# Kernel optimization log

Hardware: AMD Instinct MI355X
Metric: run time of the kernel (lower is better)

## Reference

```python
import jax, jax.numpy as jnp
import numpy as np

B, NR, NG = 16, 96, 64
AF, BF = 98, 6
H, QM, MAXNB, DEPTH = 300, 160, 10, 4
P = 2048
F = 2 * H + QM          # 760
D0 = F + 10             # 770


def _graph_idx(k, batch, n, idx_max):
    # gather_nd style indices (batch_idx, neighbor_idx): [batch, n, MAXNB, 2]
    nbr = jax.random.randint(k, (batch, n, MAXNB), 0, idx_max)
    b = jnp.broadcast_to(jnp.arange(batch)[:, None, None], (batch, n, MAXNB))
    return jnp.stack([b, nbr], axis=-1)


def setup_inputs() -> dict:
    key = jax.random.key(0)
    ks = jax.random.split(key, 32)
    f32 = jnp.float32
    inp = {}
    inp['res_atom'] = jax.random.normal(ks[0], (B, NR, AF), f32)
    inp['res_bond'] = jax.random.normal(ks[1], (B, NR, BF), f32)
    inp['res_atom_graph'] = _graph_idx(ks[2], B, NR, NR)
    inp['res_bond_graph'] = _graph_idx(ks[3], B, NR, NR)
    inp['res_num_nbs'] = jax.random.randint(ks[4], (B, NR), 1, MAXNB + 1)
    inp['res_node_mask'] = jnp.ones((B, NR, 1), f32)
    inp['rg_atom'] = jax.random.normal(ks[5], (B, NG, AF), f32)
    inp['rg_bond'] = jax.random.normal(ks[6], (B, NG, BF), f32)
    inp['rg_atom_graph'] = _graph_idx(ks[7], B, NG, NG)
    inp['rg_bond_graph'] = _graph_idx(ks[8], B, NG, NG)
    inp['rg_num_nbs'] = jax.random.randint(ks[9], (B, NG), 1, MAXNB + 1)
    inp['rg_node_mask'] = jnp.ones((B, NG, 1), f32)
    seg = jnp.repeat(jnp.arange(B), P // B)  # sorted reaction ids for segment_mean
    i = jax.random.randint(ks[10], (P,), 0, NR)
    j = jax.random.randint(ks[11], (P,), 0, NR)
    inp['core_mask'] = jnp.stack([seg, i, j], axis=-1)[None]   # [1, P, 3]
    inp['fatom_qm'] = jax.random.normal(ks[12], (B, NR, QM), f32)
    inp['connect'] = jax.random.normal(ks[13], (1, P, 10), f32)
    STD = 0.1  # keep relu chains alive at depth 4
    w = lambda k, shape: STD * jax.random.normal(k, shape, f32)
    for pre, kk in (('res', 14), ('rg', 20)):
        inp[pre + '_W_atom'] = w(ks[kk], (AF, H))
        inp[pre + '_W_nei_atom'] = w(ks[kk + 1], (H, H))
        inp[pre + '_W_nei_bond'] = w(ks[kk + 2], (BF, H))
        inp[pre + '_W_self'] = w(ks[kk + 3], (H, H))
        inp[pre + '_W_U2'] = w(ks[kk + 4], (H + BF, H))
        inp[pre + '_W_U1'] = w(ks[kk + 5], (2 * H, H))
    inp['W_att_h'] = w(ks[26], (H, H))
    inp['W_att_s'] = w(ks[27], (H, 1))
    inp['W_score0'] = 0.01 * jax.random.normal(ks[28], (D0, D0), f32)
    inp['W_score'] = 0.01 * jax.random.normal(ks[29], (D0, 1), f32)
    return inp


def _wln(atom, bond, atom_graph, bond_graph, num_nbs, node_mask,
         W_atom, W_nei_atom, W_nei_bond, W_self, W_U2, W_U1):
    relu = jax.nn.relu
    af = relu(atom @ W_atom)                                       # [B,N,H]
    mask = (jnp.arange(MAXNB)[None, None, :] < num_nbs[:, :, None])
    mask = mask.astype(af.dtype)[..., None]                        # [B,N,MAXNB,1]
    for _ in range(DEPTH):
        fa = af[atom_graph[..., 0], atom_graph[..., 1]]            # [B,N,MAXNB,H]
        fb = bond[bond_graph[..., 0], bond_graph[..., 1]]          # [B,N,MAXNB,BF]
        h_nei = relu(fa @ W_nei_atom) * relu(fb @ W_nei_bond)
        f_nei = jnp.sum(h_nei * mask, axis=2)                      # masked nbr sum
        kernels = f_nei * relu(af @ W_self) * node_mask
        pre = relu(jnp.concatenate([fa, fb], axis=3) @ W_U2)
        nei_label = jnp.sum(pre * mask, axis=2)
        af = relu(jnp.concatenate([af, nei_label], axis=2) @ W_U1)
    return kernels


def _forward(res_atom, res_bond, res_atom_graph, res_bond_graph, res_num_nbs, res_node_mask,
             rg_atom, rg_bond, rg_atom_graph, rg_bond_graph, rg_num_nbs, rg_node_mask,
             core_mask, fatom_qm, connect,
             res_W_atom, res_W_nei_atom, res_W_nei_bond, res_W_self, res_W_U2, res_W_U1,
             rg_W_atom, rg_W_nei_atom, rg_W_nei_bond, rg_W_self, rg_W_U2, rg_W_U1,
             W_att_h, W_att_s, W_score0, W_score):
    res_h = _wln(res_atom, res_bond, res_atom_graph, res_bond_graph, res_num_nbs, res_node_mask,
                 res_W_atom, res_W_nei_atom, res_W_nei_bond, res_W_self, res_W_U2, res_W_U1)
    rg_h = _wln(rg_atom, rg_bond, rg_atom_graph, rg_bond_graph, rg_num_nbs, rg_node_mask,
                rg_W_atom, rg_W_nei_atom, rg_W_nei_bond, rg_W_self, rg_W_U2, rg_W_U1)
    # Global attention: broadcast pairwise sum reactant x reagent atoms
    pair_att = res_h[:, :, None, :] + rg_h[:, None, :, :]          # [B,NR,NG,H]
    att = jax.nn.sigmoid(jax.nn.relu(pair_att @ W_att_h) @ W_att_s)
    ctx = jnp.sum(att * rg_h[:, None, :, :], axis=2)               # [B,NR,H]
    h = jnp.concatenate([res_h, ctx, fatom_qm], axis=-1)           # [B,NR,F]
    cm = core_mask[0]                                              # [P,3] = (b,i,j)
    # atom_pair[b,i,j] = h[b,i] + h[b,j]; gather only the core pairs (no N^2 tensor)
    pair = h[cm[:, 0], cm[:, 1]] + h[cm[:, 0], cm[:, 2]]           # [P,F]
    rh = jax.nn.relu(jnp.concatenate([pair, connect[0]], axis=-1) @ W_score0)
    seg = cm[:, 0]
    sums = jax.ops.segment_sum(rh, seg, num_segments=B)
    cnt = jax.ops.segment_sum(jnp.ones((P,), rh.dtype), seg, num_segments=B)
    mean = sums / cnt[:, None]                                     # segment_mean
    return mean @ W_score                                          # [B,1]


def reference(res_atom, res_bond, res_atom_graph, res_bond_graph, res_num_nbs, res_node_mask,
              rg_atom, rg_bond, rg_atom_graph, rg_bond_graph, rg_num_nbs, rg_node_mask,
              core_mask, fatom_qm, connect,
              res_W_atom, res_W_nei_atom, res_W_nei_bond, res_W_self, res_W_U2, res_W_U1,
              rg_W_atom, rg_W_nei_atom, rg_W_nei_bond, rg_W_self, rg_W_U2, rg_W_U1,
              W_att_h, W_att_s, W_score0, W_score):
    return _forward(res_atom, res_bond, res_atom_graph, res_bond_graph, res_num_nbs, res_node_mask,
                    rg_atom, rg_bond, rg_atom_graph, rg_bond_graph, rg_num_nbs, rg_node_mask,
                    core_mask, fatom_qm, connect,
                    res_W_atom, res_W_nei_atom, res_W_nei_bond, res_W_self, res_W_U2, res_W_U1,
                    rg_W_atom, rg_W_nei_atom, rg_W_nei_bond, rg_W_self, rg_W_U2, rg_W_U1,
                    W_att_h, W_att_s, W_score0, W_score)
```

## Files before the change

kernel.cpp:

```cpp
#include <hip/hip_runtime.h>


constexpr int cB = 16, cNR = 96, cNG = 64;
constexpr int cAF = 98, cBF = 6;
constexpr int cH = 300, cQM = 160, cMAXNB = 10, cDEPTH = 4;
constexpr int cP = 2048;
constexpr int cF = 2 * cH + cQM;
constexpr int cD0 = cF + 10;

constexpr int Mres = cB * cNR;
constexpr int Mrg  = cB * cNG;

typedef __attribute__((ext_vector_type(8))) short v8s;
typedef __attribute__((ext_vector_type(4))) float v4f;

__device__ inline unsigned short f2bf(float f) {
  unsigned u = __float_as_uint(f);
  u += 0x7FFF + ((u >> 16) & 1);
  return (unsigned short)(u >> 16);
}
__device__ inline float bf2f(unsigned short s) {
  return __uint_as_float(((unsigned)s) << 16);
}

struct PrepArg { const float* W; unsigned short* hiT; unsigned short* loT; int K; int N; int Kpad; };
struct PrepArgs { PrepArg a[16]; };

__global__ __launch_bounds__(256) void prep_k(PrepArgs pa)
{
  PrepArg p = pa.a[blockIdx.z];
  int idx = blockIdx.x * 256 + threadIdx.x;
  int total = p.N * p.Kpad;
  if (idx >= total) return;
  int n = idx / p.Kpad, k = idx - n * p.Kpad;
  float w = (k < p.K) ? p.W[(size_t)k * p.N + n] : 0.f;
  unsigned short h = f2bf(w);
  p.hiT[idx] = h;
  p.loT[idx] = f2bf(w - bf2f(h));
}

struct GArg {
  const float* A; const float* A2;
  const unsigned short* W1h; const unsigned short* W1l;
  const unsigned short* W2h; const unsigned short* W2l;
  float* C; int M; int K1; int Kp1; int K2; int Kp2; int act;
};
struct GArgs6 { GArg a[6]; };

#define MFMA __builtin_amdgcn_mfma_f32_16x16x32_bf16

__global__ __launch_bounds__(256) void gemm_mfma(GArgs6 ga, int N)
{
  GArg g = ga.a[blockIdx.z];
  int m0 = blockIdx.y * 64;
  if (m0 >= g.M) return;
  int n0 = blockIdx.x * 64;
  int nT = (g.Kp1 + g.Kp2) >> 5;

  __shared__ unsigned short Ah[2][64][40];
  __shared__ unsigned short Al[2][64][40];
  __shared__ unsigned short Bh[2][64][40];
  __shared__ unsigned short Bl[2][64][40];

  int tid = threadIdx.x;
  int sm = tid >> 2;
  int sk = (tid & 3) << 3;

  float areg[8];
  uint4 bh_reg, bl_reg;

  auto fetch = [&](int kv0) {
    int kv = kv0 + sk;
    const float* src; int kk, Klim;
    if (kv < g.Kp1) { src = g.A  + (size_t)(m0 + sm) * g.K1; kk = kv;          Klim = g.K1; }
    else            { src = g.A2 + (size_t)(m0 + sm) * g.K2; kk = kv - g.Kp1;  Klim = g.K2; }
    if (((Klim & 3) == 0) && kk + 7 < Klim) {
      float4 v0 = *(const float4*)(src + kk);
      float4 v1 = *(const float4*)(src + kk + 4);
      areg[0]=v0.x; areg[1]=v0.y; areg[2]=v0.z; areg[3]=v0.w;
      areg[4]=v1.x; areg[5]=v1.y; areg[6]=v1.z; areg[7]=v1.w;
    } else {
#pragma unroll
      for (int j = 0; j < 8; ++j) areg[j] = (kk + j < Klim) ? src[kk + j] : 0.f;
    }
    int gn = n0 + sm;
    if (gn < N) {
      const unsigned short *ph, *pl;
      if (kv < g.Kp1) { size_t o = (size_t)gn * g.Kp1 + kv;            ph = g.W1h + o; pl = g.W1l + o; }
      else            { size_t o = (size_t)gn * g.Kp2 + (kv - g.Kp1);  ph = g.W2h + o; pl = g.W2l + o; }
      bh_reg = *(const uint4*)ph;
      bl_reg = *(const uint4*)pl;
    } else {
      bh_reg = make_uint4(0,0,0,0); bl_reg = make_uint4(0,0,0,0);
    }
  };

  auto store = [&](int buf) {
    unsigned hs[8], ls[8];
#pragma unroll
    for (int j = 0; j < 8; ++j) {
      unsigned short h = f2bf(areg[j]);
      hs[j] = h;
      ls[j] = f2bf(areg[j] - bf2f(h));
    }
    uint4 hh, ll;
    hh.x = hs[0] | (hs[1] << 16); hh.y = hs[2] | (hs[3] << 16);
    hh.z = hs[4] | (hs[5] << 16); hh.w = hs[6] | (hs[7] << 16);
    ll.x = ls[0] | (ls[1] << 16); ll.y = ls[2] | (ls[3] << 16);
    ll.z = ls[4] | (ls[5] << 16); ll.w = ls[6] | (ls[7] << 16);
    *(uint4*)&Ah[buf][sm][sk] = hh;
    *(uint4*)&Al[buf][sm][sk] = ll;
    *(uint4*)&Bh[buf][sm][sk] = bh_reg;
    *(uint4*)&Bl[buf][sm][sk] = bl_reg;
  };

  int l = tid & 63, w = tid >> 6;
  int wm = (w >> 1) << 5, wn = (w & 1) << 5;
  int ar = wm + (l & 15), br = wn + (l & 15);
  int kc = (l >> 4) << 3;

  v4f acc00 = {0,0,0,0}, acc01 = {0,0,0,0}, acc10 = {0,0,0,0}, acc11 = {0,0,0,0};

  fetch(0); store(0); __syncthreads();
  for (int t = 0; t < nT; ++t) {
    if (t + 1 < nT) fetch((t + 1) << 5);
    int cur = t & 1;
    v8s ah0 = *(const v8s*)&Ah[cur][ar][kc];
    v8s ah1 = *(const v8s*)&Ah[cur][ar + 16][kc];
    v8s al0 = *(const v8s*)&Al[cur][ar][kc];
    v8s al1 = *(const v8s*)&Al[cur][ar + 16][kc];
    v8s bh0 = *(const v8s*)&Bh[cur][br][kc];
    v8s bh1 = *(const v8s*)&Bh[cur][br + 16][kc];
    v8s bl0 = *(const v8s*)&Bl[cur][br][kc];
    v8s bl1 = *(const v8s*)&Bl[cur][br + 16][kc];
    acc00 = MFMA(ah0, bh0, acc00, 0, 0, 0);
    acc00 = MFMA(ah0, bl0, acc00, 0, 0, 0);
    acc00 = MFMA(al0, bh0, acc00, 0, 0, 0);
    acc01 = MFMA(ah0, bh1, acc01, 0, 0, 0);
    acc01 = MFMA(ah0, bl1, acc01, 0, 0, 0);
    acc01 = MFMA(al0, bh1, acc01, 0, 0, 0);
    acc10 = MFMA(ah1, bh0, acc10, 0, 0, 0);
    acc10 = MFMA(ah1, bl0, acc10, 0, 0, 0);
    acc10 = MFMA(al1, bh0, acc10, 0, 0, 0);
    acc11 = MFMA(ah1, bh1, acc11, 0, 0, 0);
    acc11 = MFMA(ah1, bl1, acc11, 0, 0, 0);
    acc11 = MFMA(al1, bh1, acc11, 0, 0, 0);
    if (t + 1 < nT) store(cur ^ 1);
    __syncthreads();
  }

  int rbase = m0 + wm + ((l >> 4) << 2);
  int cbase = n0 + wn + (l & 15);
  auto wr = [&](v4f a, int fi, int fj) {
    int gn = cbase + fj * 16;
    if (gn >= N) return;
    float* Cp = g.C + (size_t)(rbase + fi * 16) * N + gn;
#pragma unroll
    for (int r = 0; r < 4; ++r) {
      float v = a[r];
      if (g.act) v = fmaxf(v, 0.f);
      Cp[(size_t)r * N] = v;
    }
  };
  wr(acc00, 0, 0); wr(acc01, 0, 1); wr(acc10, 1, 0); wr(acc11, 1, 1);
}

__global__ __launch_bounds__(256) void score_mfma_k(
    const float* __restrict__ h, const float* __restrict__ conn,
    const int* __restrict__ cm,
    const unsigned short* __restrict__ W0h, const unsigned short* __restrict__ W0l,
    const float* __restrict__ Wsc, float* __restrict__ pairsum)
{
  const int Kp = 800;
  const int nT = Kp >> 5;
  int m0 = blockIdx.y * 64;
  int n0 = blockIdx.x * 64;

  __shared__ unsigned short Ah[2][64][40];
  __shared__ unsigned short Al[2][64][40];
  __shared__ unsigned short Bh[2][64][40];
  __shared__ unsigned short Bl[2][64][40];

  int tid = threadIdx.x;
  int sm = tid >> 2;
  int sk = (tid & 3) << 3;

  int p = m0 + sm;
  int s3 = cm[p * 3 + 0];
  const float* h1 = h + (size_t)(s3 * cNR + cm[p * 3 + 1]) * cF;
  const float* h2 = h + (size_t)(s3 * cNR + cm[p * 3 + 2]) * cF;
  const float* cp = conn + (size_t)p * 10;

  float areg[8];
  uint4 bh_reg, bl_reg;

  auto fetch = [&](int kv0) {
    int kv = kv0 + sk;
    if (kv + 7 < cF) {
      float4 u = *(const float4*)(h1 + kv);
      float4 v = *(const float4*)(h2 + kv);
      float4 u2 = *(const float4*)(h1 + kv + 4);
      float4 v2 = *(const float4*)(h2 + kv + 4);
      areg[0]=u.x+v.x; areg[1]=u.y+v.y; areg[2]=u.z+v.z; areg[3]=u.w+v.w;
      areg[4]=u2.x+v2.x; areg[5]=u2.y+v2.y; areg[6]=u2.z+v2.z; areg[7]=u2.w+v2.w;
    } else {
#pragma unroll
      for (int j = 0; j < 8; ++j) {
        int k = kv + j;
        float v = 0.f;
        if (k < cF) v = h1[k] + h2[k];
        else if (k < cD0) v = cp[k - cF];
        areg[j] = v;
      }
    }
    int gn = n0 + sm;
    if (gn < cD0) {
      size_t o = (size_t)gn * Kp + kv;
      bh_reg = *(const uint4*)(W0h + o);
      bl_reg = *(const uint4*)(W0l + o);
    } else {
      bh_reg = make_uint4(0,0,0,0); bl_reg = make_uint4(0,0,0,0);
    }
  };

  auto store = [&](int buf) {
    unsigned hs[8], ls[8];
#pragma unroll
    for (int j = 0; j < 8; ++j) {
      unsigned short hv = f2bf(areg[j]);
      hs[j] = hv;
      ls[j] = f2bf(areg[j] - bf2f(hv));
    }
    uint4 hh, ll;
    hh.x = hs[0] | (hs[1] << 16); hh.y = hs[2] | (hs[3] << 16);
    hh.z = hs[4] | (hs[5] << 16); hh.w = hs[6] | (hs[7] << 16);
    ll.x = ls[0] | (ls[1] << 16); ll.y = ls[2] | (ls[3] << 16);
    ll.z = ls[4] | (ls[5] << 16); ll.w = ls[6] | (ls[7] << 16);
    *(uint4*)&Ah[buf][sm][sk] = hh;
    *(uint4*)&Al[buf][sm][sk] = ll;
    *(uint4*)&Bh[buf][sm][sk] = bh_reg;
    *(uint4*)&Bl[buf][sm][sk] = bl_reg;
  };

  int l = tid & 63, w = tid >> 6;
  int wm = (w >> 1) << 5, wn = (w & 1) << 5;
  int ar = wm + (l & 15), br = wn + (l & 15);
  int kc = (l >> 4) << 3;

  v4f acc00 = {0,0,0,0}, acc01 = {0,0,0,0}, acc10 = {0,0,0,0}, acc11 = {0,0,0,0};

  fetch(0); store(0); __syncthreads();
  for (int t = 0; t < nT; ++t) {
    if (t + 1 < nT) fetch((t + 1) << 5);
    int cur = t & 1;
    v8s ah0 = *(const v8s*)&Ah[cur][ar][kc];
    v8s ah1 = *(const v8s*)&Ah[cur][ar + 16][kc];
    v8s al0 = *(const v8s*)&Al[cur][ar][kc];
    v8s al1 = *(const v8s*)&Al[cur][ar + 16][kc];
    v8s bh0 = *(const v8s*)&Bh[cur][br][kc];
    v8s bh1 = *(const v8s*)&Bh[cur][br + 16][kc];
    v8s bl0 = *(const v8s*)&Bl[cur][br][kc];
    v8s bl1 = *(const v8s*)&Bl[cur][br + 16][kc];
    acc00 = MFMA(ah0, bh0, acc00, 0, 0, 0);
    acc00 = MFMA(ah0, bl0, acc00, 0, 0, 0);
    acc00 = MFMA(al0, bh0, acc00, 0, 0, 0);
    acc01 = MFMA(ah0, bh1, acc01, 0, 0, 0);
    acc01 = MFMA(ah0, bl1, acc01, 0, 0, 0);
    acc01 = MFMA(al0, bh1, acc01, 0, 0, 0);
    acc10 = MFMA(ah1, bh0, acc10, 0, 0, 0);
    acc10 = MFMA(ah1, bl0, acc10, 0, 0, 0);
    acc10 = MFMA(al1, bh0, acc10, 0, 0, 0);
    acc11 = MFMA(ah1, bh1, acc11, 0, 0, 0);
    acc11 = MFMA(ah1, bl1, acc11, 0, 0, 0);
    acc11 = MFMA(al1, bh1, acc11, 0, 0, 0);
    if (t + 1 < nT) store(cur ^ 1);
    __syncthreads();
  }

  int cbase = n0 + wn + (l & 15);
  float w0 = (cbase      < cD0) ? Wsc[cbase]      : 0.f;
  float w1 = (cbase + 16 < cD0) ? Wsc[cbase + 16] : 0.f;
  float ps[8];
#pragma unroll
  for (int r = 0; r < 4; ++r) {
    ps[r]     = fmaxf(acc00[r], 0.f) * w0 + fmaxf(acc01[r], 0.f) * w1;
    ps[4 + r] = fmaxf(acc10[r], 0.f) * w0 + fmaxf(acc11[r], 0.f) * w1;
  }
#pragma unroll
  for (int m = 1; m < 16; m <<= 1) {
#pragma unroll
    for (int q = 0; q < 8; ++q) ps[q] += __shfl_xor(ps[q], m, 64);
  }
  if ((l & 15) == 0) {
#pragma unroll
    for (int q = 0; q < 8; ++q) {
      int gm = m0 + wm + (q >> 2) * 16 + ((l >> 4) << 2) + (q & 3);
      atomicAdd(&pairsum[gm], ps[q]);
    }
  }
}

__global__ __launch_bounds__(320) void nei_label2_k(
    const float* __restrict__ RaR, const float* __restrict__ RbR,
    const int* __restrict__ agR, const int* __restrict__ bgR,
    const int* __restrict__ nnbR, float* __restrict__ outR,
    const float* __restrict__ RaG, const float* __restrict__ RbG,
    const int* __restrict__ agG, const int* __restrict__ bgG,
    const int* __restrict__ nnbG, float* __restrict__ outG)
{
  int node = blockIdx.x;
  const float *Ra, *Rb; const int *ag, *bg, *nnb; float* out; int Nn, loc;
  if (node < Mres) { Ra=RaR; Rb=RbR; ag=agR; bg=bgR; nnb=nnbR; out=outR; Nn=cNR; loc=node; }
  else { Ra=RaG; Rb=RbG; ag=agG; bg=bgG; nnb=nnbG; out=outG; Nn=cNG; loc=node-Mres; }
  int h = threadIdx.x;
  int nn = nnb[loc];
  const int* agp = ag + (size_t)loc * cMAXNB * 2;
  const int* bgp = bg + (size_t)loc * cMAXNB * 2;
  if (h < cH) {
    float s = 0.f;
    for (int k = 0; k < nn; ++k) {
      int ra = agp[2 * k] * Nn + agp[2 * k + 1];
      int rb = bgp[2 * k] * Nn + bgp[2 * k + 1];
      s += fmaxf(Ra[(size_t)ra * cH + h] + Rb[(size_t)rb * cH + h], 0.f);
    }
    out[(size_t)loc * cH + h] = s;
  }
}

__global__ __launch_bounds__(320) void kernels2_k(
    const float* __restrict__ SaR, const float* __restrict__ SbR,
    const float* __restrict__ SelfR_R,
    const int* __restrict__ agR, const int* __restrict__ bgR,
    const int* __restrict__ nnbR, const float* __restrict__ maskR,
    float* __restrict__ outR,
    const float* __restrict__ SaG, const float* __restrict__ SbG,
    const float* __restrict__ SelfR_G,
    const int* __restrict__ agG, const int* __restrict__ bgG,
    const int* __restrict__ nnbG, const float* __restrict__ maskG,
    float* __restrict__ outG)
{
  int node = blockIdx.x;
  const float *Sa, *Sb, *Se, *mk; const int *ag, *bg, *nnb; float* out; int Nn, loc;
  if (node < Mres) { Sa=SaR; Sb=SbR; Se=SelfR_R; ag=agR; bg=bgR; nnb=nnbR; mk=maskR; out=outR; Nn=cNR; loc=node; }
  else { Sa=SaG; Sb=SbG; Se=SelfR_G; ag=agG; bg=bgG; nnb=nnbG; mk=maskG; out=outG; Nn=cNG; loc=node-Mres; }
  int h = threadIdx.x;
  int nn = nnb[loc];
  const int* agp = ag + (size_t)loc * cMAXNB * 2;
  const int* bgp = bg + (size_t)loc * cMAXNB * 2;
  if (h < cH) {
    float s = 0.f;
    for (int k = 0; k < nn; ++k) {
      int ra = agp[2 * k] * Nn + agp[2 * k + 1];
      int rb = bgp[2 * k] * Nn + bgp[2 * k + 1];
      s += Sa[(size_t)ra * cH + h] * Sb[(size_t)rb * cH + h];
    }
    out[(size_t)loc * cH + h] = s * Se[(size_t)loc * cH + h] * mk[loc];
  }
}

__global__ __launch_bounds__(256) void att_ctx_h_k(
    const float* __restrict__ U, const float* __restrict__ V,
    const float* __restrict__ att_w, const float* __restrict__ rgh,
    const float* __restrict__ kern, const float* __restrict__ qm,
    float* __restrict__ h)
{
  int row = blockIdx.x;
  int b = row / cNR;
  __shared__ float Ur[cH];
  __shared__ float att[cNG];
  int tid = threadIdx.x;
  for (int n = tid; n < cH; n += 256) Ur[n] = U[(size_t)row * cH + n];
  __syncthreads();
  int wave = tid >> 6, lane = tid & 63;
  for (int j = wave; j < cNG; j += 4) {
    const float* Vr = V + (size_t)(b * cNG + j) * cH;
    float s = 0.f;
    for (int n = lane; n < cH; n += 64)
      s += fmaxf(Ur[n] + Vr[n], 0.f) * att_w[n];
    for (int off = 32; off; off >>= 1) s += __shfl_down(s, off);
    if (lane == 0) att[j] = 1.f / (1.f + expf(-s));
  }
  __syncthreads();
  float* hrow = h + (size_t)row * cF;
  for (int hh = tid; hh < cH; hh += 256) {
    float c = 0.f;
    for (int j = 0; j < cNG; ++j)
      c += att[j] * rgh[(size_t)(b * cNG + j) * cH + hh];
    hrow[cH + hh] = c;
  }
  for (int c0 = tid; c0 < cH; c0 += 256) hrow[c0] = kern[(size_t)row * cH + c0];
  for (int q0 = tid; q0 < cQM; q0 += 256) hrow[2 * cH + q0] = qm[(size_t)row * cQM + q0];
}

__global__ void seg_final_k(const float* __restrict__ ps,
                            const int* __restrict__ cm, float* __restrict__ out)
{
  __shared__ float s[cB];
  int tid = threadIdx.x;
  if (tid < cB) s[tid] = 0.f;
  __syncthreads();
  for (int p = tid; p < cP; p += 256) atomicAdd(&s[cm[p * 3]], ps[p]);
  __syncthreads();
  if (tid < cB) out[tid] = s[tid] * (1.f / 128.f);
}

extern "C" void kernel_launch(void* const* d_in, const int* in_sizes, int n_in,
                              void* d_out, int out_size, void* d_ws, size_t ws_size,
                              hipStream_t stream)
{
  (void)in_sizes; (void)n_in; (void)out_size; (void)ws_size;
  const float* res_atom = (const float*)d_in[0];
  const float* res_bond = (const float*)d_in[1];
  const int*   res_ag   = (const int*)d_in[2];
  const int*   res_bg   = (const int*)d_in[3];
  const int*   res_nnb  = (const int*)d_in[4];
  const float* res_mask = (const float*)d_in[5];
  const float* rg_atom  = (const float*)d_in[6];
  const float* rg_bond  = (const float*)d_in[7];
  const int*   rg_ag    = (const int*)d_in[8];
  const int*   rg_bg    = (const int*)d_in[9];
  const int*   rg_nnb   = (const int*)d_in[10];
  const float* rg_mask  = (const float*)d_in[11];
  const int*   core     = (const int*)d_in[12];
  const float* qm       = (const float*)d_in[13];
  const float* connect  = (const float*)d_in[14];
  const float* Wm[2][6];
  for (int s = 0; s < 2; ++s)
    for (int k = 0; k < 6; ++k) Wm[s][k] = (const float*)d_in[15 + s * 6 + k];
  const float* W_att_h  = (const float*)d_in[27];
  const float* W_att_s  = (const float*)d_in[28];
  const float* W_score0 = (const float*)d_in[29];
  const float* W_score  = (const float*)d_in[30];
  float* out = (float*)d_out;

  float* ws = (float*)d_ws;
  size_t off = 0;
  auto alloc = [&](size_t nfloat) {
    float* p = ws + off;
    off += (nfloat + 63) & ~(size_t)63;
    return p;
  };
  auto allocU = [&](size_t nush) {
    return (unsigned short*)alloc((nush + 1) / 2);
  };

  float* afA_r = alloc((size_t)Mres * cH);
  float* afB_r = alloc((size_t)Mres * cH);
  float* Rb_r  = alloc((size_t)Mres * cH);
  float* Sb_r  = alloc((size_t)Mres * cH);
  float* Ra_r  = alloc((size_t)Mres * cH);
  float* nei_r = alloc((size_t)Mres * cH);
  float* kern_r= alloc((size_t)Mres * cH);
  float* afA_g = alloc((size_t)Mrg * cH);
  float* afB_g = alloc((size_t)Mrg * cH);
  float* Rb_g  = alloc((size_t)Mrg * cH);
  float* Sb_g  = alloc((size_t)Mrg * cH);
  float* Ra_g  = alloc((size_t)Mrg * cH);
  float* nei_g = alloc((size_t)Mrg * cH);
  float* kern_g= alloc((size_t)Mrg * cH);
  float* U     = alloc((size_t)Mres * cH);
  float* V     = alloc((size_t)Mrg * cH);
  float* h760  = alloc((size_t)Mres * cF);
  float* pairsum = alloc(cP);

  struct WT { unsigned short *h, *l; int K, Kp; const float* src; };
  auto rup32 = [](int k) { return (k + 31) & ~31; };
  WT t[2][8]; 
  for (int s = 0; s < 2; ++s) {
    const int Ks[8] = {cAF, cH, cBF, cH, cH, cBF, cH, cH};
    const float* srcs[8] = {
      Wm[s][0], Wm[s][1], Wm[s][2], Wm[s][3],
      Wm[s][4], Wm[s][4] + (size_t)cH * cH,
      Wm[s][5], Wm[s][5] + (size_t)cH * cH };
    for (int k = 0; k < 8; ++k) {
      int Kp = rup32(Ks[k]);
      t[s][k].K = Ks[k]; t[s][k].Kp = Kp; t[s][k].src = srcs[k];
      t[s][k].h = allocU((size_t)cH * Kp);
      t[s][k].l = allocU((size_t)cH * Kp);
    }
  }
  unsigned short* attT_h = allocU((size_t)cH * 320);
  unsigned short* attT_l = allocU((size_t)cH * 320);
  unsigned short* sc0T_h = allocU((size_t)cD0 * 800);
  unsigned short* sc0T_l = allocU((size_t)cD0 * 800);

  {
    PrepArgs pa{};
    for (int s = 0; s < 2; ++s)
      for (int k = 0; k < 8; ++k)
        pa.a[s * 8 + k] = {t[s][k].src, t[s][k].h, t[s][k].l, t[s][k].K, cH, t[s][k].Kp};
    dim3 grid((cH * 320 + 255) / 256, 1, 16);
    prep_k<<<grid, dim3(256), 0, stream>>>(pa);
  }
  {
    PrepArgs pa{};
    pa.a[0] = {W_att_h,  attT_h, attT_l, cH, cH, 320};
    pa.a[1] = {W_score0, sc0T_h, sc0T_l, cD0, cD0, 800};
    dim3 grid((cD0 * 800 + 255) / 256, 1, 2);
    prep_k<<<grid, dim3(256), 0, stream>>>(pa);
  }

  dim3 blk(256);
  GArg zero{};
  auto launch = [&](GArgs6& ga, int nprob) {
    dim3 grid(5, Mres / 64, nprob);
    gemm_mfma<<<grid, blk, 0, stream>>>(ga, cH);
  };

  {
    GArgs6 ga{{
      {res_atom, nullptr, t[0][0].h, t[0][0].l, nullptr, nullptr, afA_r, Mres, cAF, 128, 0, 0, 1},
      {rg_atom,  nullptr, t[1][0].h, t[1][0].l, nullptr, nullptr, afA_g, Mrg,  cAF, 128, 0, 0, 1},
      {res_bond, nullptr, t[0][5].h, t[0][5].l, nullptr, nullptr, Rb_r,  Mres, cBF, 32,  0, 0, 0},
      {rg_bond,  nullptr, t[1][5].h, t[1][5].l, nullptr, nullptr, Rb_g,  Mrg,  cBF, 32,  0, 0, 0},
      {res_bond, nullptr, t[0][2].h, t[0][2].l, nullptr, nullptr, Sb_r,  Mres, cBF, 32,  0, 0, 1},
      {rg_bond,  nullptr, t[1][2].h, t[1][2].l, nullptr, nullptr, Sb_g,  Mrg,  cBF, 32,  0, 0, 1},
    }};
    launch(ga, 6);
  }

  float* af_r = afA_r; float* afo_r = afB_r;
  float* af_g = afA_g; float* afo_g = afB_g;
  for (int it = 0; it < cDEPTH - 1; ++it) {
    {
      GArgs6 ga{{
        {af_r, nullptr, t[0][4].h, t[0][4].l, nullptr, nullptr, Ra_r, Mres, cH, 320, 0, 0, 0},
        {af_g, nullptr, t[1][4].h, t[1][4].l, nullptr, nullptr, Ra_g, Mrg,  cH, 320, 0, 0, 0},
        zero, zero, zero, zero,
      }};
      launch(ga, 2);
    }
    nei_label2_k<<<dim3(Mres + Mrg), dim3(320), 0, stream>>>(
        Ra_r, Rb_r, res_ag, res_bg, res_nnb, nei_r,
        Ra_g, Rb_g, rg_ag, rg_bg, rg_nnb, nei_g);
    {
      GArgs6 ga{{
        {af_r, nei_r, t[0][6].h, t[0][6].l, t[0][7].h, t[0][7].l, afo_r, Mres, cH, 320, cH, 320, 1},
        {af_g, nei_g, t[1][6].h, t[1][6].l, t[1][7].h, t[1][7].l, afo_g, Mrg,  cH, 320, cH, 320, 1},
        zero, zero, zero, zero,
      }};
      launch(ga, 2);
    }
    { float* tmp = af_r; af_r = afo_r; afo_r = tmp; }
    { float* tmp = af_g; af_g = afo_g; afo_g = tmp; }
  }

  {
    GArgs6 ga{{
      {af_r, nullptr, t[0][1].h, t[0][1].l, nullptr, nullptr, Ra_r,  Mres, cH, 320, 0, 0, 1},
      {af_g, nullptr, t[1][1].h, t[1][1].l, nullptr, nullptr, Ra_g,  Mrg,  cH, 320, 0, 0, 1},
      {af_r, nullptr, t[0][3].h, t[0][3].l, nullptr, nullptr, nei_r, Mres, cH, 320, 0, 0, 1},
      {af_g, nullptr, t[1][3].h, t[1][3].l, nullptr, nullptr, nei_g, Mrg,  cH, 320, 0, 0, 1},
      zero, zero,
    }};
    launch(ga, 4);
  }
  kernels2_k<<<dim3(Mres + Mrg), dim3(320), 0, stream>>>(
      Ra_r, Sb_r, nei_r, res_ag, res_bg, res_nnb, res_mask, kern_r,
      Ra_g, Sb_g, nei_g, rg_ag, rg_bg, rg_nnb, rg_mask, kern_g);

  {
    GArgs6 ga{{
      {kern_r, nullptr, attT_h, attT_l, nullptr, nullptr, U, Mres, cH, 320, 0, 0, 0},
      {kern_g, nullptr, attT_h, attT_l, nullptr, nullptr, V, Mrg,  cH, 320, 0, 0, 0},
      zero, zero, zero, zero,
    }};
    launch(ga, 2);
  }
  att_ctx_h_k<<<dim3(Mres), dim3(256), 0, stream>>>(U, V, W_att_s, kern_g, kern_r, qm, h760);

  hipMemsetAsync(pairsum, 0, cP * sizeof(float), stream);
  score_mfma_k<<<dim3(13, cP / 64), blk, 0, stream>>>(
      h760, connect, core, sc0T_h, sc0T_l, W_score, pairsum);
  seg_final_k<<<dim3(1), dim3(256), 0, stream>>>(pairsum, core, out);
}
```

Before: 280.8 us.

## Tile attention-context kernel over four reactant rows per block with register reuse

The attention/context kernel now processes four residue rows per block instead of one. Each V row it loads is reused across all four U rows held in registers, and loads use float4 vectors. Partial sums are reduced with butterfly shuffles. The context matmul and the copies are vectorized, with one wave per row. This cuts redundant global loads of V and rgh, at the cost of more registers and a grid a quarter the size.

```diff
diff --git a/kernel.cpp b/kernel.cpp
--- a/kernel.cpp
+++ b/kernel.cpp
@@ -81,7 +81,10 @@
       areg[4]=v1.x; areg[5]=v1.y; areg[6]=v1.z; areg[7]=v1.w;
     } else {
 #pragma unroll
-      for (int j = 0; j < 8; ++j) areg[j] = (kk + j < Klim) ? src[kk + j] : 0.f;
+      for (int j = 0; j < 8; ++j) {
+        int k = kk + j;
+        areg[j] = (k < Klim) ? src[k] : 0.f;
+      }
     }
     int gn = n0 + sm;
     if (gn < N) {
@@ -358,38 +361,98 @@
   }
 }
 
+#define AIT 4
 __global__ __launch_bounds__(256) void att_ctx_h_k(
     const float* __restrict__ U, const float* __restrict__ V,
     const float* __restrict__ att_w, const float* __restrict__ rgh,
     const float* __restrict__ kern, const float* __restrict__ qm,
     float* __restrict__ h)
 {
-  int row = blockIdx.x;
-  int b = row / cNR;
-  __shared__ float Ur[cH];
-  __shared__ float att[cNG];
-  int tid = threadIdx.x;
-  for (int n = tid; n < cH; n += 256) Ur[n] = U[(size_t)row * cH + n];
+  __shared__ float attL[AIT][cNG];
+  int blk = blockIdx.x;
+  int b = blk / (cNR / AIT);
+  int it = blk - b * (cNR / AIT);
+  int row0 = b * cNR + it * AIT;
+  int tid = threadIdx.x, lane = tid & 63, w = tid >> 6;
+  int n0 = lane * 4, n1 = 256 + lane * 4;
+  bool v1 = (lane < 11);
+  float4 z4 = make_float4(0.f, 0.f, 0.f, 0.f);
+
+  float4 u[AIT][2], wv[2];
+  wv[0] = *(const float4*)(att_w + n0);
+  wv[1] = v1 ? *(const float4*)(att_w + n1) : z4;
+#pragma unroll
+  for (int i = 0; i < AIT; ++i) {
+    const float* Ur = U + (size_t)(row0 + i) * cH;
+    u[i][0] = *(const float4*)(Ur + n0);
+    u[i][1] = v1 ? *(const float4*)(Ur + n1) : z4;
+  }
+
+  for (int r = 0; r < 4; ++r) {
+    int jb = w * 16 + r * 4;
+    float4 vv[4][2];
+#pragma unroll
+    for (int q = 0; q < 4; ++q) {
+      const float* Vr = V + (size_t)(b * cNG + jb + q) * cH;
+      vv[q][0] = *(const float4*)(Vr + n0);
+      vv[q][1] = v1 ? *(const float4*)(Vr + n1) : z4;
+    }
+    float s[4][AIT];
+#pragma unroll
+    for (int q = 0; q < 4; ++q)
+#pragma unroll
+      for (int i = 0; i < AIT; ++i) {
+        float acc = 0.f;
+#pragma unroll
+        for (int pp = 0; pp < 2; ++pp) {
+          float4 uu = u[i][pp], vq = vv[q][pp], ww = wv[pp];
+          acc += fmaxf(uu.x + vq.x, 0.f) * ww.x;
+          acc += fmaxf(uu.y + vq.y, 0.f) * ww.y;
+          acc += fmaxf(uu.z + vq.z, 0.f) * ww.z;
+          acc += fmaxf(uu.w + vq.w, 0.f) * ww.w;
+        }
+        s[q][i] = acc;
+      }
+#pragma unroll
+    for (int m = 1; m < 64; m <<= 1)
+#pragma unroll
+      for (int q = 0; q < 4; ++q)
+#pragma unroll
+        for (int i = 0; i < AIT; ++i)
+          s[q][i] += __shfl_xor(s[q][i], m);
+    if (lane < 16) {
+      float sv = 0.f;
+#pragma unroll
+      for (int q = 0; q < 4; ++q)
+#pragma unroll
+        for (int i = 0; i < AIT; ++i)
+          if (lane == q * 4 + i) sv = s[q][i];
+      attL[lane & 3][jb + (lane >> 2)] = 1.f / (1.f + expf(-sv));
+    }
+  }
   __syncthreads();
-  int wave = tid >> 6, lane = tid & 63;
-  for (int j = wave; j < cNG; j += 4) {
-    const float* Vr = V + (size_t)(b * cNG + j) * cH;
-    float s = 0.f;
-    for (int n = lane; n < cH; n += 64)
-      s += fmaxf(Ur[n] + Vr[n], 0.f) * att_w[n];
-    for (int off = 32; off; off >>= 1) s += __shfl_down(s, off);
-    if (lane == 0) att[j] = 1.f / (1.f + expf(-s));
-  }
-  __syncthreads();
-  float* hrow = h + (size_t)row * cF;
-  for (int hh = tid; hh < cH; hh += 256) {
-    float c = 0.f;
-    for (int j = 0; j < cNG; ++j)
-      c += att[j] * rgh[(size_t)(b * cNG + j) * cH + hh];
-    hrow[cH + hh] = c;
-  }
-  for (int c0 = tid; c0 < cH; c0 += 256) hrow[c0] = kern[(size_t)row * cH + c0];
-  for (int q0 = tid; q0 < cQM; q0 += 256) hrow[2 * cH + q0] = qm[(size_t)row * cQM + q0];
+
+  const float* rgb = rgh + (size_t)b * cNG * cH;
+  float* hrow = h + (size_t)(row0 + w) * cF;
+  for (int c = lane; c < 75; c += 64) {
+    float4 p = z4;
+    for (int j = 0; j < cNG; ++j) {
+      float aj = attL[w][j];
+      float4 rv = *(const float4*)(rgb + (size_t)j * cH + c * 4);
+      p.x += aj * rv.x; p.y += aj * rv.y; p.z += aj * rv.z; p.w += aj * rv.w;
+    }
+    *(float4*)(hrow + cH + c * 4) = p;
+  }
+  for (int idx = tid; idx < AIT * 75; idx += 256) {
+    int i = idx / 75, c = idx - i * 75;
+    *(float4*)(h + (size_t)(row0 + i) * cF + c * 4) =
+        *(const float4*)(kern + (size_t)(row0 + i) * cH + c * 4);
+  }
+  for (int idx = tid; idx < AIT * 40; idx += 256) {
+    int i = idx / 40, c = idx - i * 40;
+    *(float4*)(h + (size_t)(row0 + i) * cF + 2 * cH + c * 4) =
+        *(const float4*)(qm + (size_t)(row0 + i) * cQM + c * 4);
+  }
 }
 
 __global__ void seg_final_k(const float* __restrict__ ps,
@@ -465,7 +528,7 @@
 
   struct WT { unsigned short *h, *l; int K, Kp; const float* src; };
   auto rup32 = [](int k) { return (k + 31) & ~31; };
-  WT t[2][8]; 
+  WT t[2][8];
   for (int s = 0; s < 2; ++s) {
     const int Ks[8] = {cAF, cH, cBF, cH, cH, cBF, cH, cH};
     const float* srcs[8] = {
@@ -567,7 +630,8 @@
     }};
     launch(ga, 2);
   }
-  att_ctx_h_k<<<dim3(Mres), dim3(256), 0, stream>>>(U, V, W_att_s, kern_g, kern_r, qm, h760);
+  att_ctx_h_k<<<dim3(cB * (cNR / AIT)), dim3(256), 0, stream>>>(
+      U, V, W_att_s, kern_g, kern_r, qm, h760);
 
   hipMemsetAsync(pairsum, 0, cP * sizeof(float), stream);
   score_mfma_k<<<dim3(13, cP / 64), blk, 0, stream>>>(
```

Measured after the change: 270.3 us. 1.04x faster.
